# Kernel tuning notes

Hardware: AMD Instinct MI355X
Metric: run time of the kernel (lower is better)

The kernel has to match this reference:

```python
import math
import jax, jax.numpy as jnp
import numpy as np

EMB = 512
HEADS = 8
NEG_INF = -1e30  # stand-in for -inf that stays finite under softmax


def setup_inputs() -> dict:
    key = jax.random.key(0)
    ks = jax.random.split(key, 6)
    b, t, e, h = 2, 2048, EMB, HEADS
    s = 1.0 / math.sqrt(e)
    return {
        "x": jax.random.normal(ks[0], (b, t, e), dtype=jnp.float32),
        "Wk": jax.random.normal(ks[1], (h * e, e), dtype=jnp.float32) * s,
        "Wq": jax.random.normal(ks[2], (h * e, e), dtype=jnp.float32) * s,
        "Wv": jax.random.normal(ks[3], (h * e, e), dtype=jnp.float32) * s,
        "Wc": jax.random.normal(ks[4], (e, h * e), dtype=jnp.float32) * s,
        "bc": jax.random.normal(ks[5], (e,), dtype=jnp.float32) * 0.01,
    }


def reference(x, Wk, Wq, Wv, Wc, bc):
    b, t, e = x.shape
    h = HEADS
    # projections: Linear(e, h*e) -> (b, t, h, e) -> (b, h, t, e)
    k = (x @ Wk.T).reshape(b, t, h, e).transpose(0, 2, 1, 3)
    q = (x @ Wq.T).reshape(b, t, h, e).transpose(0, 2, 1, 3)
    v = (x @ Wv.T).reshape(b, t, h, e).transpose(0, 2, 1, 3)
    scores = jnp.einsum("bhqe,bhke->bhqk", q, k) / math.sqrt(e)
    # causal mask: strict upper triangle (offset=1) set to -inf
    causal = jnp.tril(jnp.ones((t, t), dtype=bool))  # True where allowed
    scores = jnp.where(causal, scores, NEG_INF)
    weights = jax.nn.softmax(scores, axis=-1)
    out = jnp.einsum("bhqk,bhke->bhqe", weights, v)  # (b, h, t, e)
    out = out.transpose(0, 2, 1, 3).reshape(b, t, h * e)
    return out @ Wc.T + bc
```

## Files before the change

### kernel.cpp

```cpp
#include <hip/hip_runtime.h>

typedef unsigned short u16;
typedef __attribute__((ext_vector_type(4))) short short4v;
typedef __attribute__((ext_vector_type(8))) short short8;
typedef __attribute__((ext_vector_type(4))) float floatx4;

#define GLL16(g, l) __builtin_amdgcn_global_load_lds( \
    (const __attribute__((address_space(1))) void*)(g), \
    (__attribute__((address_space(3))) void*)(l), 16, 0, 0)

__device__ __forceinline__ float b2f(u16 h) {
    union { unsigned u; float f; } v; v.u = ((unsigned)h) << 16; return v.f;
}
__device__ __forceinline__ u16 f2b(float f) {
    union { float f; unsigned u; } v; v.f = f;
    unsigned r = v.u + 0x7fffu + ((v.u >> 16) & 1u);
    return (u16)(r >> 16);
}
__device__ __forceinline__ float launder(float f) {
    return fminf(fmaxf(f, -30000.0f), 30000.0f);
}

__device__ __forceinline__ int sniff_block(const u16* __restrict__ xs)
{
    __shared__ int cnt;
    if (threadIdx.x == 0) cnt = 0;
    __syncthreads();
    int local = 0;
    for (int i = threadIdx.x; i < 4096; i += 256) {
        const int ex = (xs[i] >> 7) & 0xFF;
        if (ex >= 0x90) ++local;
    }
    if (local) atomicAdd(&cnt, local);
    __syncthreads();
    return cnt > 256;
}

__device__ __forceinline__ void conv_one(const void* __restrict__ raw,
                                         u16* __restrict__ dst, int n, int isf32)
{
    int i = blockIdx.x * 256 + threadIdx.x;
    const int stride = gridDim.x * 256;
    if (isf32) {
        const float* s = (const float*)raw;
        for (; i < n; i += stride) dst[i] = f2b(s[i]);
    } else {
        const u16* s = (const u16*)raw;
        for (; i < n; i += stride) dst[i] = s[i];
    }
}

__global__ __launch_bounds__(256)
void convert4(const void* r0, const void* r1, const void* r2, const void* r3,
              u16* d0, u16* d1, u16* d2, u16* d3, int n, const u16* xs)
{
    const int isf32 = sniff_block(xs);
    const int z = blockIdx.y;
    const void* raw = (z == 0) ? r0 : (z == 1) ? r1 : (z == 2) ? r2 : r3;
    u16* dst        = (z == 0) ? d0 : (z == 1) ? d1 : (z == 2) ? d2 : d3;
    conv_one(raw, dst, n, isf32);
}

__global__ __launch_bounds__(256)
void convert2(const void* r0, const void* r1, u16* d0, u16* d1,
              int n0, int n1, const u16* xs, int* flagp)
{
    const int isf32 = sniff_block(xs);
    if (blockIdx.x == 0 && blockIdx.y == 0 && threadIdx.x == 0) flagp[0] = isf32;
    if (blockIdx.y == 0) conv_one(r0, d0, n0, isf32);
    else                 conv_one(r1, d1, n1, isf32);
}

__global__ __launch_bounds__(256, 2)
void gemm_qkv(const u16* __restrict__ A,
              const u16* __restrict__ B0, const u16* __restrict__ B1, const u16* __restrict__ B2,
              u16* __restrict__ C0, u16* __restrict__ C1, u16* __restrict__ VTout)
{
    const int z = blockIdx.z;
    const u16* B = (z == 0) ? B0 : ((z == 1) ? B1 : B2);

    __shared__ u16 As[128 * 32];
    __shared__ u16 Bs[128 * 32];

    const int tid  = threadIdx.x;
    const int wave = tid >> 6;
    const int lane = tid & 63;
    const int c16  = lane & 15;
    const int quad = lane >> 4;
    const int m0 = blockIdx.x * 128;
    const int n0 = blockIdx.y * 128;
    const int wm = (wave >> 1) * 64;
    const int wn = (wave & 1) * 64;

    floatx4 acc[4][4] = {};

    const int srow = wave * 32 + (lane >> 2);
    const int scol = (lane & 3) * 8;
    const u16* Ag = A + (size_t)(m0 + srow) * 512 + scol;
    const u16* Bg = B + (size_t)(n0 + srow) * 512 + scol;
    u16* AsW = &As[(wave * 32) * 32];
    u16* BsW = &Bs[(wave * 32) * 32];

    for (int k0 = 0; k0 < 512; k0 += 32) {
        GLL16(Ag + k0,             AsW);
        GLL16(Ag + k0 + 16 * 512,  AsW + 16 * 32);
        GLL16(Bg + k0,             BsW);
        GLL16(Bg + k0 + 16 * 512,  BsW + 16 * 32);
        __syncthreads();

        short8 af[4], bf[4];
#pragma unroll
        for (int i = 0; i < 4; ++i)
            af[i] = *(const short8*)&As[(wm + i * 16 + c16) * 32 + quad * 8];
#pragma unroll
        for (int i = 0; i < 4; ++i)
            bf[i] = *(const short8*)&Bs[(wn + i * 16 + c16) * 32 + quad * 8];
#pragma unroll
        for (int i = 0; i < 4; ++i)
#pragma unroll
            for (int j = 0; j < 4; ++j)
                acc[i][j] = __builtin_amdgcn_mfma_f32_16x16x32_bf16(af[i], bf[j], acc[i][j], 0, 0, 0);
        __syncthreads();
    }

    if (z == 2) {
#pragma unroll
        for (int i = 0; i < 4; ++i)
#pragma unroll
            for (int j = 0; j < 4; ++j) {
                const int col = n0 + wn + j * 16 + c16;
                const int hh = col >> 9, d = col & 511;
                const int rb = m0 + wm + i * 16 + quad * 4;
                const int bq = rb >> 11, tt = rb & 2047;
                short4v v4;
#pragma unroll
                for (int r = 0; r < 4; ++r) v4[r] = (short)f2b(launder(acc[i][j][r]));
                *(short4v*)&VTout[((size_t)((bq * 8 + hh) * 512 + d)) * 2048 + tt] = v4;
            }
    } else {
        u16* C = (z == 0) ? C0 : C1;
#pragma unroll
        for (int i = 0; i < 4; ++i)
#pragma unroll
            for (int j = 0; j < 4; ++j) {
                const int col = n0 + wn + j * 16 + c16;
#pragma unroll
                for (int r = 0; r < 4; ++r) {
                    const int row = m0 + wm + i * 16 + quad * 4 + r;
                    C[(size_t)row * 4096 + col] = f2b(launder(acc[i][j][r]));
                }
            }
    }
}

__global__ __launch_bounds__(256, 2)
void gemm_out(const u16* __restrict__ A, const u16* __restrict__ B,
              const u16* __restrict__ bias, const int* __restrict__ flagp,
              void* __restrict__ out)
{
    __shared__ u16 As[128 * 32];
    __shared__ u16 Bs[64 * 32];

    const int tid  = threadIdx.x;
    const int wave = tid >> 6;
    const int lane = tid & 63;
    const int c16  = lane & 15;
    const int quad = lane >> 4;
    const int m0 = blockIdx.x * 128;
    const int n0 = blockIdx.y * 64;
    const int wm = (wave >> 1) * 64;
    const int wn = (wave & 1) * 32;

    floatx4 acc[4][2] = {};

    const int srowA = wave * 32 + (lane >> 2);
    const int srowB = wave * 16 + (lane >> 2);
    const int scol  = (lane & 3) * 8;
    const u16* Ag = A + (size_t)(m0 + srowA) * 4096 + scol;
    const u16* Bg = B + (size_t)(n0 + srowB) * 4096 + scol;
    u16* AsW = &As[(wave * 32) * 32];
    u16* BsW = &Bs[(wave * 16) * 32];

    for (int k0 = 0; k0 < 4096; k0 += 32) {
        GLL16(Ag + k0,                     AsW);
        GLL16(Ag + k0 + (size_t)16 * 4096, AsW + 16 * 32);
        GLL16(Bg + k0,                     BsW);
        __syncthreads();

        short8 af[4], bf[2];
#pragma unroll
        for (int i = 0; i < 4; ++i)
            af[i] = *(const short8*)&As[(wm + i * 16 + c16) * 32 + quad * 8];
#pragma unroll
        for (int j = 0; j < 2; ++j)
            bf[j] = *(const short8*)&Bs[(wn + j * 16 + c16) * 32 + quad * 8];
#pragma unroll
        for (int i = 0; i < 4; ++i)
#pragma unroll
            for (int j = 0; j < 2; ++j)
                acc[i][j] = __builtin_amdgcn_mfma_f32_16x16x32_bf16(af[i], bf[j], acc[i][j], 0, 0, 0);
        __syncthreads();
    }

    const int isf32 = flagp[0];
#pragma unroll
    for (int i = 0; i < 4; ++i)
#pragma unroll
        for (int j = 0; j < 2; ++j) {
            const int col = n0 + wn + j * 16 + c16;
            const float bv = b2f(bias[col]);
#pragma unroll
            for (int r = 0; r < 4; ++r) {
                const int row = m0 + wm + i * 16 + quad * 4 + r;
                const float val = launder(acc[i][j][r] + bv);
                if (isf32) ((float*)out)[(size_t)row * 512 + col] = val;
                else       ((u16*)out)[(size_t)row * 512 + col] = f2b(val);
            }
        }
}

#define LOG2E 1.4426950408889634f
#define SM_SCALE 0.044194173824159216f
#define PM 24.0f

__global__ __launch_bounds__(256, 2)
void flash_attn(const u16* __restrict__ Q, const u16* __restrict__ K,
                const u16* __restrict__ VT, u16* __restrict__ O)
{
    __shared__ u16 Ks[32 * 516];
    __shared__ u16 Ps[2][16 * 36];
    __shared__ float Lp[2][2][16];

    const int tid  = threadIdx.x;
    const int wave = tid >> 6;
    const int lane = tid & 63;
    const int c16  = lane & 15;
    const int quad = lane >> 4;
    const int g  = wave & 1;
    const int st = wave >> 1;

    const int x  = blockIdx.x;
    const int bh = x & 15;
    const int pr = x >> 4;
    const int b  = bh >> 3, h = bh & 7;

    const u16* Qh  = Q  + (size_t)b * 2048 * 4096 + (size_t)h * 512;
    const u16* Kh  = K  + (size_t)b * 2048 * 4096 + (size_t)h * 512;
    const u16* VTh = VT + (size_t)bh * 512 * 2048;
    u16*       Oh  = O  + (size_t)b * 2048 * 4096 + (size_t)h * 512;

#pragma unroll
    for (int i = 0; i < 8; ++i) {
        const int kr = wave * 8 + i;
        GLL16(Kh + (size_t)kr * 4096 + lane * 8, &Ks[kr * 516]);
    }

    for (int pm = 0; pm < 2; ++pm) {
        const int qt = pm ? pr : (63 - pr);
        const int q0 = qt * 32;
        const int ntile = qt + 1;
        const int qrow = q0 + g * 16 + c16;
        const int rowq = q0 + g * 16 + quad * 4;

        short8 qf[16];
#pragma unroll
        for (int sq = 0; sq < 16; ++sq)
            qf[sq] = *(const short8*)(Qh + (size_t)qrow * 4096 + sq * 32 + quad * 8);

        float l_i[4] = {0.0f, 0.0f, 0.0f, 0.0f};
        floatx4 oacc[2][8] = {};

        for (int t = 0; t < ntile; ++t) {
            const int kv0 = t * 32;
            __syncthreads();

            floatx4 s0 = {}, s1 = {};
#pragma unroll
            for (int ks = 0; ks < 16; ks += 2) {
                short8 kf0 = *(const short8*)&Ks[(st * 16 + c16) * 516 + ks * 32 + quad * 8];
                short8 kf1 = *(const short8*)&Ks[(st * 16 + c16) * 516 + (ks + 1) * 32 + quad * 8];
                s0 = __builtin_amdgcn_mfma_f32_16x16x32_bf16(qf[ks],     kf0, s0, 0, 0, 0);
                s1 = __builtin_amdgcn_mfma_f32_16x16x32_bf16(qf[ks + 1], kf1, s1, 0, 0, 0);
            }
            const floatx4 sv = s0 + s1;

            const int col = kv0 + st * 16 + c16;
#pragma unroll
            for (int r = 0; r < 4; ++r) {
                const float pv = (col > rowq + r)
                    ? 0.0f
                    : exp2f((sv[r] * SM_SCALE - PM) * LOG2E);
                l_i[r] += pv;
                Ps[g][(quad * 4 + r) * 36 + st * 16 + c16] = f2b(pv);
            }
            __syncthreads();

            if (t + 1 < ntile || pm == 0) {
                const int knext = (t + 1 < ntile) ? (kv0 + 32) : 0;
#pragma unroll
                for (int i = 0; i < 8; ++i) {
                    const int kr = wave * 8 + i;
                    GLL16(Kh + (size_t)(knext + kr) * 4096 + lane * 8, &Ks[kr * 516]);
                }
            }

            short8 pf0 = *(const short8*)&Ps[0][c16 * 36 + quad * 8];
            short8 pf1 = *(const short8*)&Ps[1][c16 * 36 + quad * 8];
            const u16* Vw = VTh + (size_t)(wave * 128) * 2048 + kv0;
#pragma unroll
            for (int dt = 0; dt < 8; ++dt) {
                short8 vf = *(const short8*)(Vw + (size_t)(dt * 16 + c16) * 2048 + quad * 8);
                oacc[0][dt] = __builtin_amdgcn_mfma_f32_16x16x32_bf16(pf0, vf, oacc[0][dt], 0, 0, 0);
                oacc[1][dt] = __builtin_amdgcn_mfma_f32_16x16x32_bf16(pf1, vf, oacc[1][dt], 0, 0, 0);
            }
        }

#pragma unroll
        for (int off = 1; off < 16; off <<= 1)
#pragma unroll
            for (int r = 0; r < 4; ++r)
                l_i[r] += __shfl_xor(l_i[r], off, 16);
        if (c16 == 0) {
#pragma unroll
            for (int r = 0; r < 4; ++r) Lp[st][g][quad * 4 + r] = l_i[r];
        }
        __syncthreads();

#pragma unroll
        for (int gg = 0; gg < 2; ++gg) {
            float linv[4];
#pragma unroll
            for (int r = 0; r < 4; ++r)
                linv[r] = 1.0f / (Lp[0][gg][quad * 4 + r] + Lp[1][gg][quad * 4 + r]);
#pragma unroll
            for (int dt = 0; dt < 8; ++dt)
#pragma unroll
                for (int r = 0; r < 4; ++r)
                    Oh[(size_t)(q0 + gg * 16 + quad * 4 + r) * 4096 + wave * 128 + dt * 16 + c16] =
                        f2b(launder(oacc[gg][dt][r] * linv[r]));
        }
    }
}

extern "C" void kernel_launch(void* const* d_in, const int* in_sizes, int n_in,
                              void* d_out, int out_size, void* d_ws, size_t ws_size,
                              hipStream_t stream)
{
    const size_t SZ  = (size_t)4096 * 4096;
    const size_t SZh = (size_t)4096 * 512;

    u16* Qb  = (u16*)d_ws;
    u16* Kb  = Qb + SZ;
    u16* Vb  = Kb + SZ;
    u16* VTb = Vb + SZ;
    u16* Ob  = Vb;

    u16* xb  = Vb;
    u16* Wqb = Vb + SZh;
    u16* Wkb = Vb + 2 * SZh;
    u16* Wvb = Vb + 3 * SZh;

    u16* Wcb = Qb;
    u16* bcb = Qb + SZh;
    int* flagp = (int*)(Qb + 2 * SZh);

    const u16* xs = (const u16*)d_in[0];

    convert4<<<dim3(256, 4), 256, 0, stream>>>(
        d_in[0], d_in[2], d_in[1], d_in[3], xb, Wqb, Wkb, Wvb, (int)SZh, xs);

    gemm_qkv<<<dim3(32, 32, 3), 256, 0, stream>>>(
        xb, Wqb, Wkb, Wvb, Qb, Kb, VTb);

    flash_attn<<<dim3(512), 256, 0, stream>>>(Qb, Kb, VTb, Ob);

    convert2<<<dim3(256, 2), 256, 0, stream>>>(
        d_in[4], d_in[5], Wcb, bcb, (int)SZh, 512, xs, flagp);

    gemm_out<<<dim3(32, 8), 256, 0, stream>>>(Ob, Wcb, bcb, flagp, d_out);
}
```

Measured before the change: 431.7 us.

## Double-buffer K tiles in LDS and prefetch V fragments early in flash attention

Makes the K shared-memory tile double-buffered so the next tile's global-to-LDS load is issued before the current QK^T instead of after it, and loads the V fragments at the top of the iteration so their latency overlaps the score MFMAs. The causal mask is now applied only on the diagonal tile, the mid-loop __syncthreads is replaced by an explicit lgkmcnt wait plus s_barrier, and s_setprio brackets the MFMA sections. This doubles K LDS usage, which may reduce occupancy under the 2-blocks launch bound. It also holds eight V fragments live in registers and adds a barrier at the end of each pm pass.

```diff
diff --git a/kernel.cpp b/kernel.cpp
--- a/kernel.cpp
+++ b/kernel.cpp
@@ -227,7 +227,7 @@
 void flash_attn(const u16* __restrict__ Q, const u16* __restrict__ K,
                 const u16* __restrict__ VT, u16* __restrict__ O)
 {
-    __shared__ u16 Ks[32 * 516];
+    __shared__ u16 Ks[2][32 * 516];
     __shared__ u16 Ps[2][16 * 36];
     __shared__ float Lp[2][2][16];
 
@@ -236,8 +236,8 @@
     const int lane = tid & 63;
     const int c16  = lane & 15;
     const int quad = lane >> 4;
-    const int g  = wave & 1;
-    const int st = wave >> 1;
+    const int g   = wave & 1;
+    const int st2 = wave >> 1;
 
     const int x  = blockIdx.x;
     const int bh = x & 15;
@@ -252,8 +252,9 @@
 #pragma unroll
     for (int i = 0; i < 8; ++i) {
         const int kr = wave * 8 + i;
-        GLL16(Kh + (size_t)kr * 4096 + lane * 8, &Ks[kr * 516]);
-    }
+        GLL16(Kh + (size_t)kr * 4096 + lane * 8, &Ks[0][kr * 516]);
+    }
+    int cur = 0;
 
     for (int pm = 0; pm < 2; ++pm) {
         const int qt = pm ? pr : (63 - pr);
@@ -264,8 +265,8 @@
 
         short8 qf[16];
 #pragma unroll
-        for (int sq = 0; sq < 16; ++sq)
-            qf[sq] = *(const short8*)(Qh + (size_t)qrow * 4096 + sq * 32 + quad * 8);
+        for (int s = 0; s < 16; ++s)
+            qf[s] = *(const short8*)(Qh + (size_t)qrow * 4096 + s * 32 + quad * 8);
 
         float l_i[4] = {0.0f, 0.0f, 0.0f, 0.0f};
         floatx4 oacc[2][8] = {};
@@ -274,45 +275,67 @@
             const int kv0 = t * 32;
             __syncthreads();
 
-            floatx4 s0 = {}, s1 = {};
-#pragma unroll
-            for (int ks = 0; ks < 16; ks += 2) {
-                short8 kf0 = *(const short8*)&Ks[(st * 16 + c16) * 516 + ks * 32 + quad * 8];
-                short8 kf1 = *(const short8*)&Ks[(st * 16 + c16) * 516 + (ks + 1) * 32 + quad * 8];
-                s0 = __builtin_amdgcn_mfma_f32_16x16x32_bf16(qf[ks],     kf0, s0, 0, 0, 0);
-                s1 = __builtin_amdgcn_mfma_f32_16x16x32_bf16(qf[ks + 1], kf1, s1, 0, 0, 0);
-            }
-            const floatx4 sv = s0 + s1;
-
-            const int col = kv0 + st * 16 + c16;
-#pragma unroll
-            for (int r = 0; r < 4; ++r) {
-                const float pv = (col > rowq + r)
-                    ? 0.0f
-                    : exp2f((sv[r] * SM_SCALE - PM) * LOG2E);
-                l_i[r] += pv;
-                Ps[g][(quad * 4 + r) * 36 + st * 16 + c16] = f2b(pv);
-            }
-            __syncthreads();
+            short8 vf[8];
+            const u16* Vw = VTh + (size_t)(wave * 128) * 2048 + kv0;
+#pragma unroll
+            for (int dt = 0; dt < 8; ++dt)
+                vf[dt] = *(const short8*)(Vw + (size_t)(dt * 16 + c16) * 2048 + quad * 8);
 
             if (t + 1 < ntile || pm == 0) {
                 const int knext = (t + 1 < ntile) ? (kv0 + 32) : 0;
 #pragma unroll
                 for (int i = 0; i < 8; ++i) {
                     const int kr = wave * 8 + i;
-                    GLL16(Kh + (size_t)(knext + kr) * 4096 + lane * 8, &Ks[kr * 516]);
+                    GLL16(Kh + (size_t)(knext + kr) * 4096 + lane * 8,
+                          &Ks[cur ^ 1][kr * 516]);
                 }
             }
+
+            floatx4 sv0 = {}, sv1 = {};
+            __builtin_amdgcn_s_setprio(1);
+#pragma unroll
+            for (int s = 0; s < 8; ++s) {
+                short8 kf0 = *(const short8*)&Ks[cur][(st2 * 16 + c16) * 516 + s * 32 + quad * 8];
+                short8 kf1 = *(const short8*)&Ks[cur][(st2 * 16 + c16) * 516 + (s + 8) * 32 + quad * 8];
+                sv0 = __builtin_amdgcn_mfma_f32_16x16x32_bf16(qf[s],     kf0, sv0, 0, 0, 0);
+                sv1 = __builtin_amdgcn_mfma_f32_16x16x32_bf16(qf[s + 8], kf1, sv1, 0, 0, 0);
+            }
+            __builtin_amdgcn_s_setprio(0);
+            const floatx4 sv = sv0 + sv1;
+
+            const int col = kv0 + st2 * 16 + c16;
+            if (t + 1 < ntile) {
+#pragma unroll
+                for (int r = 0; r < 4; ++r) {
+                    const float p = exp2f((sv[r] * SM_SCALE - PM) * LOG2E);
+                    l_i[r] += p;
+                    Ps[g][(quad * 4 + r) * 36 + st2 * 16 + c16] = f2b(p);
+                }
+            } else {
+#pragma unroll
+                for (int r = 0; r < 4; ++r) {
+                    const float p = (col > rowq + r)
+                        ? 0.0f : exp2f((sv[r] * SM_SCALE - PM) * LOG2E);
+                    l_i[r] += p;
+                    Ps[g][(quad * 4 + r) * 36 + st2 * 16 + c16] = f2b(p);
+                }
+            }
+
+            asm volatile("s_waitcnt lgkmcnt(0)" ::: "memory");
+            __builtin_amdgcn_s_barrier();
+            __builtin_amdgcn_sched_barrier(0);
 
             short8 pf0 = *(const short8*)&Ps[0][c16 * 36 + quad * 8];
             short8 pf1 = *(const short8*)&Ps[1][c16 * 36 + quad * 8];
-            const u16* Vw = VTh + (size_t)(wave * 128) * 2048 + kv0;
+            __builtin_amdgcn_s_setprio(1);
 #pragma unroll
             for (int dt = 0; dt < 8; ++dt) {
-                short8 vf = *(const short8*)(Vw + (size_t)(dt * 16 + c16) * 2048 + quad * 8);
-                oacc[0][dt] = __builtin_amdgcn_mfma_f32_16x16x32_bf16(pf0, vf, oacc[0][dt], 0, 0, 0);
-                oacc[1][dt] = __builtin_amdgcn_mfma_f32_16x16x32_bf16(pf1, vf, oacc[1][dt], 0, 0, 0);
-            }
+                oacc[0][dt] = __builtin_amdgcn_mfma_f32_16x16x32_bf16(pf0, vf[dt], oacc[0][dt], 0, 0, 0);
+                oacc[1][dt] = __builtin_amdgcn_mfma_f32_16x16x32_bf16(pf1, vf[dt], oacc[1][dt], 0, 0, 0);
+            }
+            __builtin_amdgcn_s_setprio(0);
+
+            cur ^= 1;
         }
 
 #pragma unroll
@@ -322,7 +345,7 @@
                 l_i[r] += __shfl_xor(l_i[r], off, 16);
         if (c16 == 0) {
 #pragma unroll
-            for (int r = 0; r < 4; ++r) Lp[st][g][quad * 4 + r] = l_i[r];
+            for (int r = 0; r < 4; ++r) Lp[st2][g][quad * 4 + r] = l_i[r];
         }
         __syncthreads();
 
@@ -339,6 +362,7 @@
                     Oh[(size_t)(q0 + gg * 16 + quad * 4 + r) * 4096 + wave * 128 + dt * 16 + c16] =
                         f2b(launder(oacc[gg][dt][r] * linv[r]));
         }
+        __syncthreads();
     }
 }
 
```

Measured after the change: 416.2 us. 1.04x faster.
